# Kernel tuning notes

Measured on AMD Instinct MI355X. Metric: run time of the kernel, lower is better.

Reference implementation:

```python
import jax, jax.numpy as jnp
import numpy as np


def setup_inputs() -> dict:
    key = jax.random.key(0)
    k_x, k_adj, k_w1, k_b1, k_w2, k_b2 = jax.random.split(key, 6)
    B, S, N, HD = 16, 2048, 64, 32
    x = jax.random.normal(k_x, (B, S, N), dtype=jnp.float32)
    adj = jax.random.uniform(k_adj, (N, N), dtype=jnp.float32)
    # module forces diagonal to 1.0 at init
    adj = adj.at[jnp.arange(N), jnp.arange(N)].set(1.0)
    fc1_w = jax.random.normal(k_w1, (HD, 1), dtype=jnp.float32) * (1.0 / np.sqrt(1.0))
    fc1_b = jax.random.normal(k_b1, (HD,), dtype=jnp.float32) * 0.02
    fc2_w = jax.random.normal(k_w2, (HD, 2 * HD), dtype=jnp.float32) * (1.0 / np.sqrt(2 * HD))
    fc2_b = jax.random.normal(k_b2, (HD,), dtype=jnp.float32) * 0.02
    return {"x": x, "adj": adj, "fc1_w": fc1_w, "fc1_b": fc1_b,
            "fc2_w": fc2_w, "fc2_b": fc2_b}


def reference(x, adj, fc1_w, fc1_b, fc2_w, fc2_b):
    B, S, N = x.shape
    HD = fc1_w.shape[0]
    # row-normalized adjacency
    adj_norm = adj / (adj.sum(axis=1, keepdims=True) + 1e-8)  # [N, N]
    # fc1: Linear(1 -> HD) on x[..., None]; equivalent to outer product + bias
    h = jax.nn.relu(x[..., None] * fc1_w[:, 0] + fc1_b)       # [B, S, N, HD]
    # adjacency-weighted aggregation over variables
    agg = jnp.einsum('ij,bsjf->bsif', adj_norm, h)            # [B, S, N, HD]
    # fc2: Linear(2*HD -> HD) on concat([h, agg])
    h2 = jax.nn.relu(jnp.concatenate([h, agg], axis=-1) @ fc2_w.T + fc2_b)  # [B, S, N, HD]
    # AdaptiveAvgPool1d(1) over seq after permute(0,2,3,1).reshape(B, N*HD, S)
    z = h2.mean(axis=1).reshape(B, N * HD)                    # [B, N*HD]
    return z
```

## Files before the change

### kernel.cpp

```cpp
#include <hip/hip_runtime.h>

#define BN 16
#define SN 2048
#define NV 64
#define HD 32
#define TCH 4
#define SCHUNK 32
#define NSUB (SCHUNK / TCH)
#define CATP 36

typedef short  bf8_t  __attribute__((ext_vector_type(8)));
typedef __bf16 bfv8   __attribute__((ext_vector_type(8)));
typedef __bf16 bfv4   __attribute__((ext_vector_type(4)));
typedef float  f32x16 __attribute__((ext_vector_type(16)));

#define MFMA32(a, b, c) __builtin_amdgcn_mfma_f32_32x32x16_bf16( \
    __builtin_bit_cast(bf8_t, (a)), __builtin_bit_cast(bf8_t, (b)), (c), 0, 0, 0)

__global__ __launch_bounds__(256, 2) void gnn_mfma(
    const float* __restrict__ x,
    const float* __restrict__ adj,
    const float* __restrict__ w1,
    const float* __restrict__ b1,
    const float* __restrict__ w2,
    const float* __restrict__ b2,
    float* __restrict__ out)
{
    __shared__ __bf16 catg[TCH][NV][CATP];
    __shared__ float  red[NV * HD];
    __shared__ float  rs[NV];

    const int tid  = threadIdx.x;
    const int w    = tid >> 6;
    const int lane = tid & 63;
    const int l31  = lane & 31;
    const int lh   = lane >> 5;
    const int b    = blockIdx.x >> 6;
    const int chk  = blockIdx.x & 63;
    const int sbase = chk * SCHUNK;

    #pragma unroll
    for (int q = 0; q < (NV * HD) / 256; ++q) red[tid + q * 256] = 0.f;

    if (tid < NV) {
        float s = 0.f;
        const float4* r4 = (const float4*)(adj + tid * NV);
        #pragma unroll
        for (int q = 0; q < NV / 4; ++q) { float4 v = r4[q]; s += v.x + v.y + v.z + v.w; }
        rs[tid] = 1.f / (s + 1e-8f);
    }
    __syncthreads();

    bfv8 an[2][4];
    #pragma unroll
    for (int nt = 0; nt < 2; ++nt) {
        const int i = nt * 32 + l31;
        const float rsi = rs[i];
        #pragma unroll
        for (int kk = 0; kk < 4; ++kk) {
            const int j0 = kk * 16 + lh * 8;
            const float4 a0 = *(const float4*)(adj + i * NV + j0);
            const float4 a1 = *(const float4*)(adj + i * NV + j0 + 4);
            bfv8 v;
            v[0] = (__bf16)(a0.x * rsi); v[1] = (__bf16)(a0.y * rsi);
            v[2] = (__bf16)(a0.z * rsi); v[3] = (__bf16)(a0.w * rsi);
            v[4] = (__bf16)(a1.x * rsi); v[5] = (__bf16)(a1.y * rsi);
            v[6] = (__bf16)(a1.z * rsi); v[7] = (__bf16)(a1.w * rsi);
            an[nt][kk] = v;
        }
    }

    bfv8 wf[4];
    #pragma unroll
    for (int kk = 0; kk < 4; ++kk) {
        const int k0 = kk * 16 + lh * 8;
        const float4 a0 = *(const float4*)(w2 + l31 * (2 * HD) + k0);
        const float4 a1 = *(const float4*)(w2 + l31 * (2 * HD) + k0 + 4);
        bfv8 v;
        v[0] = (__bf16)a0.x; v[1] = (__bf16)a0.y; v[2] = (__bf16)a0.z; v[3] = (__bf16)a0.w;
        v[4] = (__bf16)a1.x; v[5] = (__bf16)a1.y; v[6] = (__bf16)a1.z; v[7] = (__bf16)a1.w;
        wf[kk] = v;
    }

    const float w1f = w1[l31];
    const float b1f = b1[l31];
    const float b2f = b2[l31];
    float w1k[2][8], b1k[2][8];
    #pragma unroll
    for (int kk = 0; kk < 2; ++kk) {
        const int k0 = kk * 16 + lh * 8;
        #pragma unroll
        for (int e = 0; e < 8; ++e) { w1k[kk][e] = w1[k0 + e]; b1k[kk][e] = b1[k0 + e]; }
    }

    f32x16 macc0, macc1;
    #pragma unroll
    for (int r = 0; r < 16; ++r) { macc0[r] = 0.f; macc1[r] = 0.f; }

    for (int t = 0; t < NSUB; ++t) {
        const float* xp = x + ((size_t)b * SN + sbase + t * TCH + w) * (size_t)NV;

        bfv8 a1f[4];
        #pragma unroll
        for (int kk = 0; kk < 4; ++kk) {
            const int j0 = kk * 16 + lh * 8;
            const float4 xa = *(const float4*)(xp + j0);
            const float4 xb = *(const float4*)(xp + j0 + 4);
            bfv8 v;
            v[0] = (__bf16)fmaxf(xa.x * w1f + b1f, 0.f);
            v[1] = (__bf16)fmaxf(xa.y * w1f + b1f, 0.f);
            v[2] = (__bf16)fmaxf(xa.z * w1f + b1f, 0.f);
            v[3] = (__bf16)fmaxf(xa.w * w1f + b1f, 0.f);
            v[4] = (__bf16)fmaxf(xb.x * w1f + b1f, 0.f);
            v[5] = (__bf16)fmaxf(xb.y * w1f + b1f, 0.f);
            v[6] = (__bf16)fmaxf(xb.z * w1f + b1f, 0.f);
            v[7] = (__bf16)fmaxf(xb.w * w1f + b1f, 0.f);
            a1f[kk] = v;
        }
        #pragma unroll
        for (int nt = 0; nt < 2; ++nt) {
            f32x16 c;
            #pragma unroll
            for (int r = 0; r < 16; ++r) c[r] = 0.f;
            #pragma unroll
            for (int kk = 0; kk < 4; ++kk) c = MFMA32(a1f[kk], an[nt][kk], c);
            const int i = nt * 32 + l31;
            #pragma unroll
            for (int g = 0; g < 4; ++g) {
                const int f0 = g * 8 + 4 * lh;
                bfv4 pv;
                pv[0] = (__bf16)c[g * 4 + 0]; pv[1] = (__bf16)c[g * 4 + 1];
                pv[2] = (__bf16)c[g * 4 + 2]; pv[3] = (__bf16)c[g * 4 + 3];
                *(bfv4*)&catg[w][i][f0] = pv;
            }
        }

        #pragma unroll
        for (int p = 0; p < 2; ++p) {
            const int ih = p;
            const int i  = ih * 32 + l31;
            const float xv = xp[i];
            f32x16 c;
            #pragma unroll
            for (int r = 0; r < 16; ++r) c[r] = 0.f;
            #pragma unroll
            for (int kk = 0; kk < 2; ++kk) {
                bfv8 v;
                #pragma unroll
                for (int e = 0; e < 8; ++e)
                    v[e] = (__bf16)fmaxf(xv * w1k[kk][e] + b1k[kk][e], 0.f);
                c = MFMA32(v, wf[kk], c);
            }
            #pragma unroll
            for (int kk = 2; kk < 4; ++kk) {
                const int f0 = (kk - 2) * 16 + lh * 8;
                const bfv4 lo = *(const bfv4*)&catg[w][i][f0];
                const bfv4 hi = *(const bfv4*)&catg[w][i][f0 + 4];
                bfv8 v;
                #pragma unroll
                for (int e = 0; e < 4; ++e) { v[e] = lo[e]; v[e + 4] = hi[e]; }
                c = MFMA32(v, wf[kk], c);
            }
            #pragma unroll
            for (int r = 0; r < 16; ++r) {
                const float h2 = fmaxf(c[r] + b2f, 0.f);
                if (p == 0) macc0[r] += h2; else macc1[r] += h2;
            }
        }
    }

    #pragma unroll
    for (int r = 0; r < 16; ++r) {
        const int row = (r & 3) + 8 * (r >> 2) + 4 * lh;
        atomicAdd(&red[row * HD + l31], macc0[r]);
        atomicAdd(&red[(row + 32) * HD + l31], macc1[r]);
    }
    __syncthreads();
    const float inv = 1.f / (float)SN;
    #pragma unroll
    for (int q = 0; q < (NV * HD) / 256; ++q) {
        const int e = tid + q * 256;
        atomicAdd(out + (size_t)b * (NV * HD) + e, red[e] * inv);
    }
}

extern "C" void kernel_launch(void* const* d_in, const int* in_sizes, int n_in,
                              void* d_out, int out_size, void* d_ws, size_t ws_size,
                              hipStream_t stream) {
    const float* x   = (const float*)d_in[0];
    const float* adj = (const float*)d_in[1];
    const float* w1  = (const float*)d_in[2];
    const float* b1  = (const float*)d_in[3];
    const float* w2  = (const float*)d_in[4];
    const float* b2  = (const float*)d_in[5];
    float* out = (float*)d_out;

    hipMemsetAsync(out, 0, (size_t)out_size * sizeof(float), stream);
    gnn_mfma<<<dim3(BN * 64), dim3(256), 0, stream>>>(x, adj, w1, b1, w2, b2, out);
}
```

Measured before the change: 142.3 us.

## Keep aggregation tile in registers via lane shuffles instead of LDS round trip

The aggregation MFMA result is packed to bf16 and rearranged across the two half-waves with xor shuffles, so it can feed the fc2 MFMA directly as the B operand. This removes the shared-memory staging buffer and its writes and reads. The fc2 MFMA operands are swapped so the output is laid out feature by node, which needs a per-row bias vector and a transposed reduction buffer. Adjacency row sums are now computed per lane with a shuffle instead of a block barrier, and launch bounds move to three blocks per CU. The cost is extra shuffle and packing instructions and more register pressure per thread.

After: 238.4 us. 67.5% more time.

```diff
diff --git a/kernel.cpp b/kernel.cpp
--- a/kernel.cpp
+++ b/kernel.cpp
@@ -4,20 +4,38 @@
 #define SN 2048
 #define NV 64
 #define HD 32
-#define TCH 4
 #define SCHUNK 32
-#define NSUB (SCHUNK / TCH)
-#define CATP 36
+#define NSUB 8
 
 typedef short  bf8_t  __attribute__((ext_vector_type(8)));
 typedef __bf16 bfv8   __attribute__((ext_vector_type(8)));
-typedef __bf16 bfv4   __attribute__((ext_vector_type(4)));
 typedef float  f32x16 __attribute__((ext_vector_type(16)));
+typedef int    i32x4  __attribute__((ext_vector_type(4)));
 
 #define MFMA32(a, b, c) __builtin_amdgcn_mfma_f32_32x32x16_bf16( \
     __builtin_bit_cast(bf8_t, (a)), __builtin_bit_cast(bf8_t, (b)), (c), 0, 0, 0)
 
-__global__ __launch_bounds__(256, 2) void gnn_mfma(
+static __device__ __forceinline__ int pack2bf(float lo, float hi) {
+    const unsigned short a = __builtin_bit_cast(unsigned short, (__bf16)lo);
+    const unsigned short b = __builtin_bit_cast(unsigned short, (__bf16)hi);
+    return (int)a | ((int)b << 16);
+}
+
+static __device__ __forceinline__ void make_bagg(
+    const f32x16& c, const int lh, i32x4& B2, i32x4& B3)
+{
+    int d[8], p[8];
+    #pragma unroll
+    for (int q = 0; q < 8; ++q) d[q] = pack2bf(c[2 * q], c[2 * q + 1]);
+    #pragma unroll
+    for (int q = 0; q < 8; ++q) p[q] = __shfl_xor(d[q], 32);
+    B2 = (i32x4){ lh ? p[2] : d[0], lh ? p[3] : d[1],
+                  lh ? d[2] : p[0], lh ? d[3] : p[1] };
+    B3 = (i32x4){ lh ? p[6] : d[4], lh ? p[7] : d[5],
+                  lh ? d[6] : p[4], lh ? d[7] : p[5] };
+}
+
+__global__ __launch_bounds__(256, 3) void gnn_mfma(
     const float* __restrict__ x,
     const float* __restrict__ adj,
     const float* __restrict__ w1,
@@ -26,9 +44,7 @@
     const float* __restrict__ b2,
     float* __restrict__ out)
 {
-    __shared__ __bf16 catg[TCH][NV][CATP];
-    __shared__ float  red[NV * HD];
-    __shared__ float  rs[NV];
+    __shared__ float red[HD * NV];
 
     const int tid  = threadIdx.x;
     const int w    = tid >> 6;
@@ -42,30 +58,28 @@
     #pragma unroll
     for (int q = 0; q < (NV * HD) / 256; ++q) red[tid + q * 256] = 0.f;
 
-    if (tid < NV) {
-        float s = 0.f;
-        const float4* r4 = (const float4*)(adj + tid * NV);
-        #pragma unroll
-        for (int q = 0; q < NV / 4; ++q) { float4 v = r4[q]; s += v.x + v.y + v.z + v.w; }
-        rs[tid] = 1.f / (s + 1e-8f);
-    }
-    __syncthreads();
-
     bfv8 an[2][4];
     #pragma unroll
     for (int nt = 0; nt < 2; ++nt) {
         const int i = nt * 32 + l31;
-        const float rsi = rs[i];
+        float av[4][8];
+        float psum = 0.f;
         #pragma unroll
         for (int kk = 0; kk < 4; ++kk) {
             const int j0 = kk * 16 + lh * 8;
             const float4 a0 = *(const float4*)(adj + i * NV + j0);
             const float4 a1 = *(const float4*)(adj + i * NV + j0 + 4);
+            av[kk][0] = a0.x; av[kk][1] = a0.y; av[kk][2] = a0.z; av[kk][3] = a0.w;
+            av[kk][4] = a1.x; av[kk][5] = a1.y; av[kk][6] = a1.z; av[kk][7] = a1.w;
+            psum += a0.x + a0.y + a0.z + a0.w + a1.x + a1.y + a1.z + a1.w;
+        }
+        const float fullsum = psum + __shfl_xor(psum, 32);
+        const float rsi = 1.f / (fullsum + 1e-8f);
+        #pragma unroll
+        for (int kk = 0; kk < 4; ++kk) {
             bfv8 v;
-            v[0] = (__bf16)(a0.x * rsi); v[1] = (__bf16)(a0.y * rsi);
-            v[2] = (__bf16)(a0.z * rsi); v[3] = (__bf16)(a0.w * rsi);
-            v[4] = (__bf16)(a1.x * rsi); v[5] = (__bf16)(a1.y * rsi);
-            v[6] = (__bf16)(a1.z * rsi); v[7] = (__bf16)(a1.w * rsi);
+            #pragma unroll
+            for (int e = 0; e < 8; ++e) v[e] = (__bf16)(av[kk][e] * rsi);
             an[nt][kk] = v;
         }
     }
@@ -84,7 +98,6 @@
 
     const float w1f = w1[l31];
     const float b1f = b1[l31];
-    const float b2f = b2[l31];
     float w1k[2][8], b1k[2][8];
     #pragma unroll
     for (int kk = 0; kk < 2; ++kk) {
@@ -92,13 +105,16 @@
         #pragma unroll
         for (int e = 0; e < 8; ++e) { w1k[kk][e] = w1[k0 + e]; b1k[kk][e] = b1[k0 + e]; }
     }
+    float b2r[16];
+    #pragma unroll
+    for (int r = 0; r < 16; ++r) b2r[r] = b2[(r & 3) + 8 * (r >> 2) + 4 * lh];
 
     f32x16 macc0, macc1;
     #pragma unroll
     for (int r = 0; r < 16; ++r) { macc0[r] = 0.f; macc1[r] = 0.f; }
 
     for (int t = 0; t < NSUB; ++t) {
-        const float* xp = x + ((size_t)b * SN + sbase + t * TCH + w) * (size_t)NV;
+        const float* xp = x + ((size_t)b * SN + sbase + t * 4 + w) * (size_t)NV;
 
         bfv8 a1f[4];
         #pragma unroll
@@ -117,29 +133,21 @@
             v[7] = (__bf16)fmaxf(xb.w * w1f + b1f, 0.f);
             a1f[kk] = v;
         }
+        const float xv0 = xp[l31];
+        const float xv1 = xp[32 + l31];
+
         #pragma unroll
         for (int nt = 0; nt < 2; ++nt) {
-            f32x16 c;
-            #pragma unroll
-            for (int r = 0; r < 16; ++r) c[r] = 0.f;
-            #pragma unroll
-            for (int kk = 0; kk < 4; ++kk) c = MFMA32(a1f[kk], an[nt][kk], c);
-            const int i = nt * 32 + l31;
-            #pragma unroll
-            for (int g = 0; g < 4; ++g) {
-                const int f0 = g * 8 + 4 * lh;
-                bfv4 pv;
-                pv[0] = (__bf16)c[g * 4 + 0]; pv[1] = (__bf16)c[g * 4 + 1];
-                pv[2] = (__bf16)c[g * 4 + 2]; pv[3] = (__bf16)c[g * 4 + 3];
-                *(bfv4*)&catg[w][i][f0] = pv;
-            }
-        }
-
-        #pragma unroll
-        for (int p = 0; p < 2; ++p) {
-            const int ih = p;
-            const int i  = ih * 32 + l31;
-            const float xv = xp[i];
+            f32x16 c1;
+            #pragma unroll
+            for (int r = 0; r < 16; ++r) c1[r] = 0.f;
+            #pragma unroll
+            for (int kk = 0; kk < 4; ++kk) c1 = MFMA32(a1f[kk], an[nt][kk], c1);
+
+            i32x4 B2, B3;
+            make_bagg(c1, lh, B2, B3);
+
+            const float xv = (nt == 0) ? xv0 : xv1;
             f32x16 c;
             #pragma unroll
             for (int r = 0; r < 16; ++r) c[r] = 0.f;
@@ -149,38 +157,32 @@
                 #pragma unroll
                 for (int e = 0; e < 8; ++e)
                     v[e] = (__bf16)fmaxf(xv * w1k[kk][e] + b1k[kk][e], 0.f);
-                c = MFMA32(v, wf[kk], c);
+                c = MFMA32(wf[kk], v, c);
             }
-            #pragma unroll
-            for (int kk = 2; kk < 4; ++kk) {
-                const int f0 = (kk - 2) * 16 + lh * 8;
-                const bfv4 lo = *(const bfv4*)&catg[w][i][f0];
-                const bfv4 hi = *(const bfv4*)&catg[w][i][f0 + 4];
-                bfv8 v;
-                #pragma unroll
-                for (int e = 0; e < 4; ++e) { v[e] = lo[e]; v[e + 4] = hi[e]; }
-                c = MFMA32(v, wf[kk], c);
+            c = MFMA32(wf[2], B2, c);
+            c = MFMA32(wf[3], B3, c);
+            #pragma unroll
+            for (int r = 0; r < 16; ++r) {
+                const float h2 = fmaxf(c[r] + b2r[r], 0.f);
+                if (nt == 0) macc0[r] += h2; else macc1[r] += h2;
             }
-            #pragma unroll
-            for (int r = 0; r < 16; ++r) {
-                const float h2 = fmaxf(c[r] + b2f, 0.f);
-                if (p == 0) macc0[r] += h2; else macc1[r] += h2;
-            }
-        }
-    }
-
+        }
+    }
+
+    __syncthreads();
     #pragma unroll
     for (int r = 0; r < 16; ++r) {
-        const int row = (r & 3) + 8 * (r >> 2) + 4 * lh;
-        atomicAdd(&red[row * HD + l31], macc0[r]);
-        atomicAdd(&red[(row + 32) * HD + l31], macc1[r]);
+        const int fr = (r & 3) + 8 * (r >> 2) + 4 * lh;
+        atomicAdd(&red[fr * NV + l31],      macc0[r]);
+        atomicAdd(&red[fr * NV + 32 + l31], macc1[r]);
     }
     __syncthreads();
     const float inv = 1.f / (float)SN;
     #pragma unroll
     for (int q = 0; q < (NV * HD) / 256; ++q) {
         const int e = tid + q * 256;
-        atomicAdd(out + (size_t)b * (NV * HD) + e, red[e] * inv);
+        const int i = e & 63, f = e >> 6;
+        atomicAdd(out + (size_t)b * (NV * HD) + i * HD + f, red[e] * inv);
     }
 }
 
```

## Process two timesteps per wave, alias LDS buffers, compute row sums in registers

Applied to the files above, without the earlier changes.

Each wave now handles two sequence steps per iteration (TCH 8), which halves the outer loop trip count and gives more independent MFMA work per iteration. The aggregation buffer and the reduction buffer now share LDS through a union, and the adjacency row sums are computed in registers with a cross-half-wave shuffle instead of a shared-memory pass plus a barrier. Launch bounds are raised to ask for 3 blocks per CU. The extra in-flight state raises register pressure, which may conflict with the higher occupancy target, and the aliased LDS needs additional barriers at the end.

Result: slower. 158.8 us (+11.6%).

```diff
diff --git a/kernel.cpp b/kernel.cpp
--- a/kernel.cpp
+++ b/kernel.cpp
@@ -4,7 +4,7 @@
 #define SN 2048
 #define NV 64
 #define HD 32
-#define TCH 4
+#define TCH 8
 #define SCHUNK 32
 #define NSUB (SCHUNK / TCH)
 #define CATP 36
@@ -17,7 +17,7 @@
 #define MFMA32(a, b, c) __builtin_amdgcn_mfma_f32_32x32x16_bf16( \
     __builtin_bit_cast(bf8_t, (a)), __builtin_bit_cast(bf8_t, (b)), (c), 0, 0, 0)
 
-__global__ __launch_bounds__(256, 2) void gnn_mfma(
+__global__ __launch_bounds__(256, 3) void gnn_mfma(
     const float* __restrict__ x,
     const float* __restrict__ adj,
     const float* __restrict__ w1,
@@ -26,9 +26,10 @@
     const float* __restrict__ b2,
     float* __restrict__ out)
 {
-    __shared__ __bf16 catg[TCH][NV][CATP];
-    __shared__ float  red[NV * HD];
-    __shared__ float  rs[NV];
+    __shared__ union SMem {
+        __bf16 catg[TCH][NV][CATP];
+        float  red[NV * HD];
+    } sm;
 
     const int tid  = threadIdx.x;
     const int w    = tid >> 6;
@@ -39,33 +40,28 @@
     const int chk  = blockIdx.x & 63;
     const int sbase = chk * SCHUNK;
 
-    #pragma unroll
-    for (int q = 0; q < (NV * HD) / 256; ++q) red[tid + q * 256] = 0.f;
-
-    if (tid < NV) {
-        float s = 0.f;
-        const float4* r4 = (const float4*)(adj + tid * NV);
-        #pragma unroll
-        for (int q = 0; q < NV / 4; ++q) { float4 v = r4[q]; s += v.x + v.y + v.z + v.w; }
-        rs[tid] = 1.f / (s + 1e-8f);
-    }
-    __syncthreads();
-
     bfv8 an[2][4];
     #pragma unroll
     for (int nt = 0; nt < 2; ++nt) {
         const int i = nt * 32 + l31;
-        const float rsi = rs[i];
+        float av[4][8];
+        float psum = 0.f;
         #pragma unroll
         for (int kk = 0; kk < 4; ++kk) {
             const int j0 = kk * 16 + lh * 8;
             const float4 a0 = *(const float4*)(adj + i * NV + j0);
             const float4 a1 = *(const float4*)(adj + i * NV + j0 + 4);
+            av[kk][0] = a0.x; av[kk][1] = a0.y; av[kk][2] = a0.z; av[kk][3] = a0.w;
+            av[kk][4] = a1.x; av[kk][5] = a1.y; av[kk][6] = a1.z; av[kk][7] = a1.w;
+            psum += a0.x + a0.y + a0.z + a0.w + a1.x + a1.y + a1.z + a1.w;
+        }
+        const float fullsum = psum + __shfl_xor(psum, 32);
+        const float rsi = 1.f / (fullsum + 1e-8f);
+        #pragma unroll
+        for (int kk = 0; kk < 4; ++kk) {
             bfv8 v;
-            v[0] = (__bf16)(a0.x * rsi); v[1] = (__bf16)(a0.y * rsi);
-            v[2] = (__bf16)(a0.z * rsi); v[3] = (__bf16)(a0.w * rsi);
-            v[4] = (__bf16)(a1.x * rsi); v[5] = (__bf16)(a1.y * rsi);
-            v[6] = (__bf16)(a1.z * rsi); v[7] = (__bf16)(a1.w * rsi);
+            #pragma unroll
+            for (int e = 0; e < 8; ++e) v[e] = (__bf16)(av[kk][e] * rsi);
             an[nt][kk] = v;
         }
     }
@@ -98,48 +94,56 @@
     for (int r = 0; r < 16; ++r) { macc0[r] = 0.f; macc1[r] = 0.f; }
 
     for (int t = 0; t < NSUB; ++t) {
-        const float* xp = x + ((size_t)b * SN + sbase + t * TCH + w) * (size_t)NV;
-
-        bfv8 a1f[4];
-        #pragma unroll
-        for (int kk = 0; kk < 4; ++kk) {
-            const int j0 = kk * 16 + lh * 8;
-            const float4 xa = *(const float4*)(xp + j0);
-            const float4 xb = *(const float4*)(xp + j0 + 4);
-            bfv8 v;
-            v[0] = (__bf16)fmaxf(xa.x * w1f + b1f, 0.f);
-            v[1] = (__bf16)fmaxf(xa.y * w1f + b1f, 0.f);
-            v[2] = (__bf16)fmaxf(xa.z * w1f + b1f, 0.f);
-            v[3] = (__bf16)fmaxf(xa.w * w1f + b1f, 0.f);
-            v[4] = (__bf16)fmaxf(xb.x * w1f + b1f, 0.f);
-            v[5] = (__bf16)fmaxf(xb.y * w1f + b1f, 0.f);
-            v[6] = (__bf16)fmaxf(xb.z * w1f + b1f, 0.f);
-            v[7] = (__bf16)fmaxf(xb.w * w1f + b1f, 0.f);
-            a1f[kk] = v;
-        }
-        #pragma unroll
-        for (int nt = 0; nt < 2; ++nt) {
-            f32x16 c;
-            #pragma unroll
-            for (int r = 0; r < 16; ++r) c[r] = 0.f;
-            #pragma unroll
-            for (int kk = 0; kk < 4; ++kk) c = MFMA32(a1f[kk], an[nt][kk], c);
-            const int i = nt * 32 + l31;
-            #pragma unroll
-            for (int g = 0; g < 4; ++g) {
-                const int f0 = g * 8 + 4 * lh;
-                bfv4 pv;
-                pv[0] = (__bf16)c[g * 4 + 0]; pv[1] = (__bf16)c[g * 4 + 1];
-                pv[2] = (__bf16)c[g * 4 + 2]; pv[3] = (__bf16)c[g * 4 + 3];
-                *(bfv4*)&catg[w][i][f0] = pv;
-            }
-        }
-
-        #pragma unroll
-        for (int p = 0; p < 2; ++p) {
-            const int ih = p;
+        const float* xp0 = x + ((size_t)b * SN + sbase + t * TCH + 2 * w) * (size_t)NV;
+        const float* xp1 = xp0 + NV;
+
+        #pragma unroll
+        for (int sp = 0; sp < 2; ++sp) {
+            const float* xp = sp ? xp1 : xp0;
+            const int sl = 2 * w + sp;
+            bfv8 a1f[4];
+            #pragma unroll
+            for (int kk = 0; kk < 4; ++kk) {
+                const int j0 = kk * 16 + lh * 8;
+                const float4 xa = *(const float4*)(xp + j0);
+                const float4 xb = *(const float4*)(xp + j0 + 4);
+                bfv8 v;
+                v[0] = (__bf16)fmaxf(xa.x * w1f + b1f, 0.f);
+                v[1] = (__bf16)fmaxf(xa.y * w1f + b1f, 0.f);
+                v[2] = (__bf16)fmaxf(xa.z * w1f + b1f, 0.f);
+                v[3] = (__bf16)fmaxf(xa.w * w1f + b1f, 0.f);
+                v[4] = (__bf16)fmaxf(xb.x * w1f + b1f, 0.f);
+                v[5] = (__bf16)fmaxf(xb.y * w1f + b1f, 0.f);
+                v[6] = (__bf16)fmaxf(xb.z * w1f + b1f, 0.f);
+                v[7] = (__bf16)fmaxf(xb.w * w1f + b1f, 0.f);
+                a1f[kk] = v;
+            }
+            #pragma unroll
+            for (int nt = 0; nt < 2; ++nt) {
+                f32x16 c;
+                #pragma unroll
+                for (int r = 0; r < 16; ++r) c[r] = 0.f;
+                #pragma unroll
+                for (int kk = 0; kk < 4; ++kk) c = MFMA32(a1f[kk], an[nt][kk], c);
+                const int i = nt * 32 + l31;
+                #pragma unroll
+                for (int g = 0; g < 4; ++g) {
+                    const int f0 = g * 8 + 4 * lh;
+                    bfv4 pv;
+                    pv[0] = (__bf16)c[g * 4 + 0]; pv[1] = (__bf16)c[g * 4 + 1];
+                    pv[2] = (__bf16)c[g * 4 + 2]; pv[3] = (__bf16)c[g * 4 + 3];
+                    *(bfv4*)&sm.catg[sl][i][f0] = pv;
+                }
+            }
+        }
+
+        #pragma unroll
+        for (int p = 0; p < 4; ++p) {
+            const int sp = p >> 1;
+            const int sl = 2 * w + sp;
+            const int ih = p & 1;
             const int i  = ih * 32 + l31;
-            const float xv = xp[i];
+            const float xv = (sp ? xp1 : xp0)[i];
             f32x16 c;
             #pragma unroll
             for (int r = 0; r < 16; ++r) c[r] = 0.f;
@@ -154,8 +158,8 @@
             #pragma unroll
             for (int kk = 2; kk < 4; ++kk) {
                 const int f0 = (kk - 2) * 16 + lh * 8;
-                const bfv4 lo = *(const bfv4*)&catg[w][i][f0];
-                const bfv4 hi = *(const bfv4*)&catg[w][i][f0 + 4];
+                const bfv4 lo = *(const bfv4*)&sm.catg[sl][i][f0];
+                const bfv4 hi = *(const bfv4*)&sm.catg[sl][i][f0 + 4];
                 bfv8 v;
                 #pragma unroll
                 for (int e = 0; e < 4; ++e) { v[e] = lo[e]; v[e + 4] = hi[e]; }
@@ -164,23 +168,27 @@
             #pragma unroll
             for (int r = 0; r < 16; ++r) {
                 const float h2 = fmaxf(c[r] + b2f, 0.f);
-                if (p == 0) macc0[r] += h2; else macc1[r] += h2;
-            }
-        }
-    }
-
+                if (ih == 0) macc0[r] += h2; else macc1[r] += h2;
+            }
+        }
+    }
+
+    __syncthreads();
+    #pragma unroll
+    for (int q = 0; q < (NV * HD) / 256; ++q) sm.red[tid + q * 256] = 0.f;
+    __syncthreads();
     #pragma unroll
     for (int r = 0; r < 16; ++r) {
         const int row = (r & 3) + 8 * (r >> 2) + 4 * lh;
-        atomicAdd(&red[row * HD + l31], macc0[r]);
-        atomicAdd(&red[(row + 32) * HD + l31], macc1[r]);
+        atomicAdd(&sm.red[row * HD + l31], macc0[r]);
+        atomicAdd(&sm.red[(row + 32) * HD + l31], macc1[r]);
     }
     __syncthreads();
     const float inv = 1.f / (float)SN;
     #pragma unroll
     for (int q = 0; q < (NV * HD) / 256; ++q) {
         const int e = tid + q * 256;
-        atomicAdd(out + (size_t)b * (NV * HD) + e, red[e] * inv);
+        atomicAdd(out + (size_t)b * (NV * HD) + e, sm.red[e] * inv);
     }
 }
 
```
